# Optimization experiments

Measured on AMD Instinct MI355X. Metric: run time of the kernel, lower is better.

The kernel has to match this reference:

```python
import jax, jax.numpy as jnp
import numpy as np

N = 32768        # batch of sampled sequences
H = 1024         # LSTM hidden (cell) size
P = 128          # proj_size == output_size == operator_length
IN = 2 * (P + 1) + 4 + 1  # 263 = 2*(operator_length+1) + scatter_max_degree + 1
SOFT = 64        # soft_length
TSS = 16.0       # two_sigma_square
AZB, AZE = 0, 32    # operators.arity_zero_begin/end (token layout assumption)
A2B, A2E = 96, 128  # operators.arity_two_begin/end


def setup_inputs() -> dict:
    key = jax.random.key(0)
    ks = jax.random.split(key, 16)
    s = 0.05
    inp = {
        "input": jax.random.normal(ks[0], (N, IN), jnp.float32),
        "hidden": jax.random.normal(ks[1], (2, N, H), jnp.float32),       # c-state
        "hidden_lstm": jax.random.normal(ks[2], (2, N, P), jnp.float32),  # h-state (proj)
        # layer 0 (input -> H, projected to P)
        "W_ih0": jax.random.normal(ks[3], (4 * H, IN), jnp.float32) * s,
        "W_hh0": jax.random.normal(ks[4], (4 * H, P), jnp.float32) * s,
        "b_ih0": jax.random.normal(ks[5], (4 * H,), jnp.float32) * s,
        "b_hh0": jax.random.normal(ks[6], (4 * H,), jnp.float32) * s,
        "W_hr0": jax.random.normal(ks[7], (P, H), jnp.float32) * s,
        # layer 1 (P -> H, projected to P)
        "W_ih1": jax.random.normal(ks[8], (4 * H, P), jnp.float32) * s,
        "W_hh1": jax.random.normal(ks[9], (4 * H, P), jnp.float32) * s,
        "b_ih1": jax.random.normal(ks[10], (4 * H,), jnp.float32) * s,
        "b_hh1": jax.random.normal(ks[11], (4 * H,), jnp.float32) * s,
        "W_hr1": jax.random.normal(ks[12], (P, H), jnp.float32) * s,
        "cur_length": 10,
    }
    return inp


def lstm_cell(x, h, c, Wih, Whh, bih, bhh, Whr):
    # PyTorch gate order: i, f, g, o ; proj_size projection via Whr
    gates = x @ Wih.T + h @ Whh.T + (bih + bhh)   # [n, 4H]
    i, f, g, o = jnp.split(gates, 4, axis=-1)
    c_new = jax.nn.sigmoid(f) * c + jax.nn.sigmoid(i) * jnp.tanh(g)
    h_new = (jax.nn.sigmoid(o) * jnp.tanh(c_new)) @ Whr.T  # project H -> P
    return h_new, c_new


def reference(input, hidden, hidden_lstm,
              W_ih0, W_hh0, b_ih0, b_hh0, W_hr0,
              W_ih1, W_hh1, b_ih1, b_hh1, W_hr1,
              cur_length):
    h0, c0 = lstm_cell(input, hidden_lstm[0], hidden[0], W_ih0, W_hh0, b_ih0, b_hh0, W_hr0)
    h1, c1 = lstm_cell(h0, hidden_lstm[1], hidden[1], W_ih1, W_hh1, b_ih1, b_hh1, W_hr1)
    # prior bias (cur_length is a static Python int)
    prior = jnp.zeros((P,), jnp.float32)
    if cur_length < SOFT:
        prior = prior.at[AZB:AZE].set(-float(SOFT - cur_length) ** 2 / TSS)
    elif cur_length > SOFT:
        prior = prior.at[A2B:A2E].set(-float(cur_length - SOFT) ** 2 / TSS)
    out = jax.nn.softmax(h1 + prior[None, :], axis=1)  # [n, P]
    cn = jnp.stack([c0, c1])  # [2, n, H]
    hn = jnp.stack([h0, h1])  # [2, n, P]
    return out, cn, hn
```

## Files before the change

kernel.cpp:

```cpp
#include <hip/hip_runtime.h>
#include <stdint.h>

#define NB 32768
#define HH 1024
#define PP 128
#define INW 263
#define K0P 448
#define K1P 256
#define G4H 4096

typedef __attribute__((ext_vector_type(8))) short short8;
typedef __attribute__((ext_vector_type(4))) float floatx4;

__device__ __forceinline__ unsigned short f2bf(float x) {
    union { float f; unsigned int u; } v; v.f = x;
    unsigned int r = v.u + 0x7fffu + ((v.u >> 16) & 1u);
    return (unsigned short)(r >> 16);
}
__device__ __forceinline__ float sigm(float x) { return 1.f / (1.f + __expf(-x)); }
__device__ __forceinline__ float tanhfast(float x) { return 2.f / (1.f + __expf(-2.f * x)) - 1.f; }

__device__ __forceinline__ void load_lds16(const void* g, void* l) {
    __builtin_amdgcn_global_load_lds((const __attribute__((address_space(1))) void*)g,
                                     (__attribute__((address_space(3))) void*)l,
                                     16, 0, 0);
}

__global__ void prep_inputs(const float* __restrict__ inp, const float* __restrict__ hl,
                            unsigned short* __restrict__ X0, unsigned short* __restrict__ X1) {
    const int T0 = NB * K0P;
    const int T1 = T0 + NB * PP;
    for (int idx = blockIdx.x * 256 + threadIdx.x; idx < T1; idx += gridDim.x * 256) {
        if (idx < T0) {
            int n = idx / K0P, c = idx - n * K0P;
            float v = 0.f;
            if (c < INW) v = inp[n * INW + c];
            else if (c < INW + PP) v = hl[n * PP + (c - INW)];
            X0[idx] = f2bf(v);
        } else {
            int k = idx - T0;
            int n = k >> 7, c = k & 127;
            X1[n * K1P + PP + c] = f2bf(hl[NB * PP + k]);
        }
    }
}

__global__ void prep_weights(const float* __restrict__ Wih0, const float* __restrict__ Whh0,
                             const float* __restrict__ Wih1, const float* __restrict__ Whh1,
                             const float* __restrict__ Whr0, const float* __restrict__ Whr1,
                             const float* __restrict__ bih0, const float* __restrict__ bhh0,
                             const float* __restrict__ bih1, const float* __restrict__ bhh1,
                             unsigned short* __restrict__ Wp0, unsigned short* __restrict__ Wp1,
                             unsigned short* __restrict__ Whr0b, unsigned short* __restrict__ Whr1b,
                             float* __restrict__ b0, float* __restrict__ b1) {
    const int T0 = G4H * K0P;
    const int T1 = T0 + G4H * K1P;
    const int T2 = T1 + PP * HH;
    const int T3 = T2 + PP * HH;
    const int T4 = T3 + G4H;
    const int T5 = T4 + G4H;
    for (int idx = blockIdx.x * 256 + threadIdx.x; idx < T5; idx += gridDim.x * 256) {
        if (idx < T0) {
            int r = idx / K0P, c = idx - r * K0P;
            int cbb = r >> 7, tt = r & 127;
            int src = (tt >> 5) * 1024 + cbb * 32 + (tt & 31);
            float v = 0.f;
            if (c < INW) v = Wih0[src * INW + c];
            else if (c < INW + PP) v = Whh0[src * PP + (c - INW)];
            Wp0[idx] = f2bf(v);
        } else if (idx < T1) {
            int k = idx - T0;
            int r = k >> 8, c = k & 255;
            int cbb = r >> 7, tt = r & 127;
            int src = (tt >> 5) * 1024 + cbb * 32 + (tt & 31);
            float v = (c < PP) ? Wih1[src * PP + c] : Whh1[src * PP + (c - PP)];
            Wp1[k] = f2bf(v);
        } else if (idx < T2) {
            int k = idx - T1; Whr0b[k] = f2bf(Whr0[k]);
        } else if (idx < T3) {
            int k = idx - T2; Whr1b[k] = f2bf(Whr1[k]);
        } else if (idx < T4) {
            int k = idx - T3; b0[k] = bih0[k] + bhh0[k];
        } else {
            int k = idx - T4; b1[k] = bih1[k] + bhh1[k];
        }
    }
}

template<int KPAD>
__global__ __launch_bounds__(256, 2) void gemm_gates_k(
    const unsigned short* __restrict__ A,
    const unsigned short* __restrict__ Bp,
    const float* __restrict__ bias,
    const float* __restrict__ c_prev,
    float* __restrict__ c_out,
    unsigned short* __restrict__ tmp_out)
{
    __shared__ unsigned short As[128 * 64];
    __shared__ unsigned short Bs[128 * 64];
    const int t  = threadIdx.x;
    const int w  = t >> 6;
    const int l  = t & 63;
    const int lc = l & 15;
    const int q4 = l >> 4;
    const int cb = blockIdx.x;
    const int mb = blockIdx.y;

    floatx4 acc[2][8];
#pragma unroll
    for (int i = 0; i < 2; ++i)
#pragma unroll
        for (int j = 0; j < 8; ++j) acc[i][j] = (floatx4){0.f, 0.f, 0.f, 0.f};

    const int arow = t >> 3;
    const int sw   = ((t & 7) ^ ((t >> 3) & 7)) * 8;
    const unsigned short* gA = A  + (size_t)(mb * 128 + arow) * KPAD + sw;
    const unsigned short* gB = Bp + (size_t)(cb * 128 + arow) * KPAD + sw;
    char* ldsA = (char*)As + t * 16;
    char* ldsB = (char*)Bs + t * 16;

    for (int kt = 0; kt < KPAD; kt += 64) {
#pragma unroll
        for (int i = 0; i < 4; ++i) {
            load_lds16(gA + (size_t)(i * 32) * KPAD + kt, ldsA + i * 4096);
            load_lds16(gB + (size_t)(i * 32) * KPAD + kt, ldsB + i * 4096);
        }
        __syncthreads();
        const short* Asp = (const short*)As;
        const short* Bsp = (const short*)Bs;
#pragma unroll
        for (int kc = 0; kc < 2; ++kc) {
            const int kchunk = kc * 4 + q4;
            const int rsw = (kchunk ^ (lc & 7)) * 8;
            short8 a[2];
#pragma unroll
            for (int mi = 0; mi < 2; ++mi)
                a[mi] = *(const short8*)&Asp[(w * 32 + mi * 16 + lc) * 64 + rsw];
#pragma unroll
            for (int ci = 0; ci < 8; ++ci) {
                short8 b = *(const short8*)&Bsp[(ci * 16 + lc) * 64 + rsw];
#pragma unroll
                for (int mi = 0; mi < 2; ++mi)
                    acc[mi][ci] = __builtin_amdgcn_mfma_f32_16x16x32_bf16(a[mi], b, acc[mi][ci], 0, 0, 0);
            }
        }
        __syncthreads();
    }

#pragma unroll
    for (int u4 = 0; u4 < 2; ++u4) {
        const int hidx = cb * 32 + u4 * 16 + lc;
        const float bi = bias[hidx];
        const float bf = bias[1024 + hidx];
        const float bg = bias[2048 + hidx];
        const float bo = bias[3072 + hidx];
#pragma unroll
        for (int mi = 0; mi < 2; ++mi) {
#pragma unroll
            for (int r = 0; r < 4; ++r) {
                const int row = mb * 128 + w * 32 + mi * 16 + q4 * 4 + r;
                const float iv = acc[mi][0 + u4][r] + bi;
                const float fv = acc[mi][2 + u4][r] + bf;
                const float gv = acc[mi][4 + u4][r] + bg;
                const float ov = acc[mi][6 + u4][r] + bo;
                const float cp = c_prev[(size_t)row * 1024 + hidx];
                const float cn = sigm(fv) * cp + sigm(iv) * tanhfast(gv);
                c_out[(size_t)row * 1024 + hidx] = cn;
                tmp_out[(size_t)row * 1024 + hidx] = f2bf(sigm(ov) * tanhfast(cn));
            }
        }
    }
}

__global__ __launch_bounds__(256, 2) void gemm_proj_k(
    const unsigned short* __restrict__ A,
    const unsigned short* __restrict__ B,
    float* __restrict__ hout,
    unsigned short* __restrict__ xc1)
{
    __shared__ unsigned short As[128 * 64];
    __shared__ unsigned short Bs[128 * 64];
    const int t  = threadIdx.x;
    const int w  = t >> 6;
    const int l  = t & 63;
    const int lc = l & 15;
    const int q4 = l >> 4;
    const int mb = blockIdx.x;

    floatx4 acc[2][8];
#pragma unroll
    for (int i = 0; i < 2; ++i)
#pragma unroll
        for (int j = 0; j < 8; ++j) acc[i][j] = (floatx4){0.f, 0.f, 0.f, 0.f};

    const int arow = t >> 3;
    const int sw   = ((t & 7) ^ ((t >> 3) & 7)) * 8;
    const unsigned short* gA = A + (size_t)(mb * 128 + arow) * 1024 + sw;
    const unsigned short* gB = B + (size_t)arow * 1024 + sw;
    char* ldsA = (char*)As + t * 16;
    char* ldsB = (char*)Bs + t * 16;

    for (int kt = 0; kt < 1024; kt += 64) {
#pragma unroll
        for (int i = 0; i < 4; ++i) {
            load_lds16(gA + (size_t)(i * 32) * 1024 + kt, ldsA + i * 4096);
            load_lds16(gB + (size_t)(i * 32) * 1024 + kt, ldsB + i * 4096);
        }
        __syncthreads();
        const short* Asp = (const short*)As;
        const short* Bsp = (const short*)Bs;
#pragma unroll
        for (int kc = 0; kc < 2; ++kc) {
            const int kchunk = kc * 4 + q4;
            const int rsw = (kchunk ^ (lc & 7)) * 8;
            short8 a[2];
#pragma unroll
            for (int mi = 0; mi < 2; ++mi)
                a[mi] = *(const short8*)&Asp[(w * 32 + mi * 16 + lc) * 64 + rsw];
#pragma unroll
            for (int ci = 0; ci < 8; ++ci) {
                short8 b = *(const short8*)&Bsp[(ci * 16 + lc) * 64 + rsw];
#pragma unroll
                for (int mi = 0; mi < 2; ++mi)
                    acc[mi][ci] = __builtin_amdgcn_mfma_f32_16x16x32_bf16(a[mi], b, acc[mi][ci], 0, 0, 0);
            }
        }
        __syncthreads();
    }

#pragma unroll
    for (int ci = 0; ci < 8; ++ci) {
        const int col = ci * 16 + lc;
#pragma unroll
        for (int mi = 0; mi < 2; ++mi) {
#pragma unroll
            for (int r = 0; r < 4; ++r) {
                const int row = mb * 128 + w * 32 + mi * 16 + q4 * 4 + r;
                const float v = acc[mi][ci][r];
                hout[(size_t)row * 128 + col] = v;
                if (xc1) xc1[(size_t)row * K1P + col] = f2bf(v);
            }
        }
    }
}

__global__ void softmax_k(const float* __restrict__ h1, const int* __restrict__ clp,
                          float* __restrict__ out) {
    const int w = threadIdx.x >> 6, l = threadIdx.x & 63;
    const int row = blockIdx.x * 4 + w;
    const int cl = clp[0];
    float pd = 0.f;
    float d = (float)(64 - cl);
    float pv = -(d * d) * (1.f / 16.f);
    float p0 = (cl < 64 && l < 32) ? pv : 0.f;
    float p1 = (cl > 64 && (l + 64) >= 96) ? pv : 0.f;
    (void)pd;
    float v0 = h1[(size_t)row * 128 + l] + p0;
    float v1 = h1[(size_t)row * 128 + 64 + l] + p1;
    float m = fmaxf(v0, v1);
#pragma unroll
    for (int off = 32; off > 0; off >>= 1) m = fmaxf(m, __shfl_xor(m, off, 64));
    float e0 = __expf(v0 - m), e1 = __expf(v1 - m);
    float s = e0 + e1;
#pragma unroll
    for (int off = 32; off > 0; off >>= 1) s += __shfl_xor(s, off, 64);
    float inv = 1.f / s;
    out[(size_t)row * 128 + l] = e0 * inv;
    out[(size_t)row * 128 + 64 + l] = e1 * inv;
}

extern "C" void kernel_launch(void* const* d_in, const int* in_sizes, int n_in,
                              void* d_out, int out_size, void* d_ws, size_t ws_size,
                              hipStream_t stream) {
    const float* input = (const float*)d_in[0];
    const float* hidden = (const float*)d_in[1];
    const float* hlstm  = (const float*)d_in[2];
    const float* Wih0 = (const float*)d_in[3];
    const float* Whh0 = (const float*)d_in[4];
    const float* bih0 = (const float*)d_in[5];
    const float* bhh0 = (const float*)d_in[6];
    const float* Whr0 = (const float*)d_in[7];
    const float* Wih1 = (const float*)d_in[8];
    const float* Whh1 = (const float*)d_in[9];
    const float* bih1 = (const float*)d_in[10];
    const float* bhh1 = (const float*)d_in[11];
    const float* Whr1 = (const float*)d_in[12];
    const int* curlen = (const int*)d_in[13];

    float* out = (float*)d_out;
    float* cn0 = out + (size_t)NB * PP;
    float* cn1 = cn0 + (size_t)NB * HH;
    float* hn0 = cn1 + (size_t)NB * HH;
    float* hn1 = hn0 + (size_t)NB * PP;

    char* p = (char*)d_ws;
    unsigned short* X0    = (unsigned short*)p; p += (size_t)NB * K0P * 2;
    unsigned short* X1    = (unsigned short*)p; p += (size_t)NB * K1P * 2;
    unsigned short* Wp0   = (unsigned short*)p; p += (size_t)G4H * K0P * 2;
    unsigned short* Wp1   = (unsigned short*)p; p += (size_t)G4H * K1P * 2;
    unsigned short* Whr0b = (unsigned short*)p; p += (size_t)PP * HH * 2;
    unsigned short* Whr1b = (unsigned short*)p; p += (size_t)PP * HH * 2;
    float* b0 = (float*)p; p += (size_t)G4H * 4;
    float* b1 = (float*)p; p += (size_t)G4H * 4;
    unsigned short* tmp0 = (unsigned short*)p; p += (size_t)NB * HH * 2;
    unsigned short* tmp1 = (unsigned short*)p; p += (size_t)NB * HH * 2;

    prep_inputs<<<8192, 256, 0, stream>>>(input, hlstm, X0, X1);
    prep_weights<<<4096, 256, 0, stream>>>(Wih0, Whh0, Wih1, Whh1, Whr0, Whr1,
                                           bih0, bhh0, bih1, bhh1,
                                           Wp0, Wp1, Whr0b, Whr1b, b0, b1);
    gemm_gates_k<K0P><<<dim3(32, 256), 256, 0, stream>>>(X0, Wp0, b0, hidden, cn0, tmp0);
    gemm_proj_k<<<256, 256, 0, stream>>>(tmp0, Whr0b, hn0, X1);
    gemm_gates_k<K1P><<<dim3(32, 256), 256, 0, stream>>>(X1, Wp1, b1, hidden + (size_t)NB * HH, cn1, tmp1);
    gemm_proj_k<<<256, 256, 0, stream>>>(tmp1, Whr1b, hn1, nullptr);
    softmax_k<<<NB / 4, 256, 0, stream>>>(hn1, curlen, out);
}
```

Measured before the change: 913.8 us.

## Triple-buffer GEMM K-loops, enlarge gate tiles, shrink proj tiles, restructure prep kernels

The gate GEMM now uses 256x128 tiles and a 3-stage ring of 32-wide K slices, waiting on vmcnt instead of a full barrier, so global loads overlap MFMA work. It also prefetches c_prev and bias before the last K steps. The projection GEMM drops to 64-row tiles (512 blocks) with the same 3-stage pipeline to give more blocks for parallelism. The prep kernels switch from flat grid-stride indexing with divisions to per-row blocks. The cost is higher register and LDS pressure from the 4x8 accumulators, and the hand-written waitcnt counts must stay exactly in step with the number of loads issued per stage.

Result: no change. 906.9 us (-0.8%).

```diff
diff --git a/kernel.cpp b/kernel.cpp
--- a/kernel.cpp
+++ b/kernel.cpp
@@ -28,19 +28,19 @@
 
 __global__ void prep_inputs(const float* __restrict__ inp, const float* __restrict__ hl,
                             unsigned short* __restrict__ X0, unsigned short* __restrict__ X1) {
-    const int T0 = NB * K0P;
-    const int T1 = T0 + NB * PP;
-    for (int idx = blockIdx.x * 256 + threadIdx.x; idx < T1; idx += gridDim.x * 256) {
-        if (idx < T0) {
-            int n = idx / K0P, c = idx - n * K0P;
+    const int n0 = blockIdx.x * 4;
+#pragma unroll
+    for (int rr = 0; rr < 4; ++rr) {
+        const int n = n0 + rr;
+        for (int c = threadIdx.x; c < K0P; c += 256) {
             float v = 0.f;
             if (c < INW) v = inp[n * INW + c];
             else if (c < INW + PP) v = hl[n * PP + (c - INW)];
-            X0[idx] = f2bf(v);
-        } else {
-            int k = idx - T0;
-            int n = k >> 7, c = k & 127;
-            X1[n * K1P + PP + c] = f2bf(hl[NB * PP + k]);
+            X0[(size_t)n * K0P + c] = f2bf(v);
+        }
+        if (threadIdx.x < PP) {
+            const int c = threadIdx.x;
+            X1[(size_t)n * K1P + PP + c] = f2bf(hl[(size_t)NB * PP + n * PP + c]);
         }
     }
 }
@@ -53,37 +53,29 @@
                              unsigned short* __restrict__ Wp0, unsigned short* __restrict__ Wp1,
                              unsigned short* __restrict__ Whr0b, unsigned short* __restrict__ Whr1b,
                              float* __restrict__ b0, float* __restrict__ b1) {
-    const int T0 = G4H * K0P;
-    const int T1 = T0 + G4H * K1P;
-    const int T2 = T1 + PP * HH;
-    const int T3 = T2 + PP * HH;
-    const int T4 = T3 + G4H;
-    const int T5 = T4 + G4H;
-    for (int idx = blockIdx.x * 256 + threadIdx.x; idx < T5; idx += gridDim.x * 256) {
-        if (idx < T0) {
-            int r = idx / K0P, c = idx - r * K0P;
-            int cbb = r >> 7, tt = r & 127;
-            int src = (tt >> 5) * 1024 + cbb * 32 + (tt & 31);
-            float v = 0.f;
-            if (c < INW) v = Wih0[src * INW + c];
-            else if (c < INW + PP) v = Whh0[src * PP + (c - INW)];
-            Wp0[idx] = f2bf(v);
-        } else if (idx < T1) {
-            int k = idx - T0;
-            int r = k >> 8, c = k & 255;
-            int cbb = r >> 7, tt = r & 127;
-            int src = (tt >> 5) * 1024 + cbb * 32 + (tt & 31);
-            float v = (c < PP) ? Wih1[src * PP + c] : Whh1[src * PP + (c - PP)];
-            Wp1[k] = f2bf(v);
-        } else if (idx < T2) {
-            int k = idx - T1; Whr0b[k] = f2bf(Whr0[k]);
-        } else if (idx < T3) {
-            int k = idx - T2; Whr1b[k] = f2bf(Whr1[k]);
-        } else if (idx < T4) {
-            int k = idx - T3; b0[k] = bih0[k] + bhh0[k];
-        } else {
-            int k = idx - T4; b1[k] = bih1[k] + bhh1[k];
-        }
+    const int b = blockIdx.x;
+    const int cbb = b >> 7, tt = b & 127;
+    const int src = (tt >> 5) * 1024 + cbb * 32 + (tt & 31);
+    for (int c = threadIdx.x; c < K0P; c += 256) {
+        float v = 0.f;
+        if (c < INW) v = Wih0[src * INW + c];
+        else if (c < INW + PP) v = Whh0[src * PP + (c - INW)];
+        Wp0[(size_t)b * K0P + c] = f2bf(v);
+    }
+    for (int c = threadIdx.x; c < K1P; c += 256) {
+        float v = (c < PP) ? Wih1[src * PP + c] : Whh1[src * PP + (c - PP)];
+        Wp1[(size_t)b * K1P + c] = f2bf(v);
+    }
+    if (b < PP) {
+        for (int c = threadIdx.x; c < HH; c += 256) {
+            Whr0b[b * HH + c] = f2bf(Whr0[b * HH + c]);
+            Whr1b[b * HH + c] = f2bf(Whr1[b * HH + c]);
+        }
+    }
+    if (b < 16) {
+        const int k = b * 256 + threadIdx.x;
+        b0[k] = bih0[k] + bhh0[k];
+        b1[k] = bih1[k] + bhh1[k];
     }
 }
 
@@ -96,8 +88,8 @@
     float* __restrict__ c_out,
     unsigned short* __restrict__ tmp_out)
 {
-    __shared__ unsigned short As[128 * 64];
-    __shared__ unsigned short Bs[128 * 64];
+    __shared__ unsigned short As[3 * 256 * 32];
+    __shared__ unsigned short Bs[3 * 128 * 32];
     const int t  = threadIdx.x;
     const int w  = t >> 6;
     const int l  = t & 63;
@@ -106,64 +98,99 @@
     const int cb = blockIdx.x;
     const int mb = blockIdx.y;
 
-    floatx4 acc[2][8];
-#pragma unroll
-    for (int i = 0; i < 2; ++i)
+    floatx4 acc[4][8];
+#pragma unroll
+    for (int i = 0; i < 4; ++i)
 #pragma unroll
         for (int j = 0; j < 8; ++j) acc[i][j] = (floatx4){0.f, 0.f, 0.f, 0.f};
 
-    const int arow = t >> 3;
-    const int sw   = ((t & 7) ^ ((t >> 3) & 7)) * 8;
-    const unsigned short* gA = A  + (size_t)(mb * 128 + arow) * KPAD + sw;
-    const unsigned short* gB = Bp + (size_t)(cb * 128 + arow) * KPAD + sw;
-    char* ldsA = (char*)As + t * 16;
-    char* ldsB = (char*)Bs + t * 16;
-
-    for (int kt = 0; kt < KPAD; kt += 64) {
-#pragma unroll
-        for (int i = 0; i < 4; ++i) {
-            load_lds16(gA + (size_t)(i * 32) * KPAD + kt, ldsA + i * 4096);
-            load_lds16(gB + (size_t)(i * 32) * KPAD + kt, ldsB + i * 4096);
-        }
-        __syncthreads();
-        const short* Asp = (const short*)As;
-        const short* Bsp = (const short*)Bs;
-#pragma unroll
-        for (int kc = 0; kc < 2; ++kc) {
-            const int kchunk = kc * 4 + q4;
-            const int rsw = (kchunk ^ (lc & 7)) * 8;
-            short8 a[2];
-#pragma unroll
-            for (int mi = 0; mi < 2; ++mi)
-                a[mi] = *(const short8*)&Asp[(w * 32 + mi * 16 + lc) * 64 + rsw];
-#pragma unroll
-            for (int ci = 0; ci < 8; ++ci) {
-                short8 b = *(const short8*)&Bsp[(ci * 16 + lc) * 64 + rsw];
-#pragma unroll
-                for (int mi = 0; mi < 2; ++mi)
-                    acc[mi][ci] = __builtin_amdgcn_mfma_f32_16x16x32_bf16(a[mi], b, acc[mi][ci], 0, 0, 0);
+    const int ar = t >> 2;
+    const int aj = (t & 3) ^ ((t >> 3) & 3);
+    const unsigned short* gA = A  + (size_t)(mb * 256 + ar) * KPAD + aj * 8;
+    const unsigned short* gB = Bp + (size_t)(cb * 128 + ar) * KPAD + aj * 8;
+    char* lA = (char*)As + t * 16;
+    char* lB = (char*)Bs + t * 16;
+
+#define GSTAGE(buf, kte) do {                                                       \
+    _Pragma("unroll") for (int i_ = 0; i_ < 4; ++i_)                                \
+        load_lds16(gA + (size_t)(i_ * 64) * KPAD + (kte), lA + (buf) * 16384 + i_ * 4096); \
+    _Pragma("unroll") for (int i_ = 0; i_ < 2; ++i_)                                \
+        load_lds16(gB + (size_t)(i_ * 64) * KPAD + (kte), lB + (buf) * 8192 + i_ * 4096);  \
+} while (0)
+
+    constexpr int NT = KPAD / 32;
+
+    GSTAGE(0, 0);
+    GSTAGE(1, 32);
+    GSTAGE(2, 64);
+
+    float cpv[4][2][4];
+    float bv[2][4];
+
+#pragma unroll
+    for (int ki = 0; ki < NT; ++ki) {
+        if (ki < NT - 2)       asm volatile("s_waitcnt vmcnt(12)" ::: "memory");
+        else if (ki == NT - 2) asm volatile("s_waitcnt vmcnt(6)" ::: "memory");
+        else                   asm volatile("s_waitcnt vmcnt(0)" ::: "memory");
+
+        if (ki == NT - 2) {
+#pragma unroll
+            for (int u4 = 0; u4 < 2; ++u4) {
+                const int hidx = cb * 32 + u4 * 16 + lc;
+#pragma unroll
+                for (int j = 0; j < 4; ++j) bv[u4][j] = bias[j * 1024 + hidx];
+#pragma unroll
+                for (int mi = 0; mi < 4; ++mi)
+#pragma unroll
+                    for (int r = 0; r < 4; ++r)
+                        cpv[mi][u4][r] =
+                            c_prev[(size_t)(mb * 256 + w * 64 + mi * 16 + q4 * 4 + r) * 1024 + hidx];
             }
         }
-        __syncthreads();
-    }
+
+        __builtin_amdgcn_s_barrier();
+        asm volatile("" ::: "memory");
+
+        const short* Asp = (const short*)As + (ki % 3) * 8192;
+        const short* Bsp = (const short*)Bs + (ki % 3) * 4096;
+        const int pos8 = (q4 ^ ((lc >> 1) & 3)) * 8;
+        short8 a[4];
+#pragma unroll
+        for (int mi = 0; mi < 4; ++mi)
+            a[mi] = *(const short8*)&Asp[(w * 64 + mi * 16 + lc) * 32 + pos8];
+#pragma unroll
+        for (int ci = 0; ci < 8; ++ci) {
+            short8 b = *(const short8*)&Bsp[(ci * 16 + lc) * 32 + pos8];
+#pragma unroll
+            for (int mi = 0; mi < 4; ++mi)
+                acc[mi][ci] = __builtin_amdgcn_mfma_f32_16x16x32_bf16(a[mi], b, acc[mi][ci], 0, 0, 0);
+        }
+
+        if (ki + 3 < NT) {
+            asm volatile("" ::: "memory");
+            __builtin_amdgcn_s_barrier();
+            GSTAGE(ki % 3, (ki + 3) * 32);
+        }
+    }
+#undef GSTAGE
 
 #pragma unroll
     for (int u4 = 0; u4 < 2; ++u4) {
         const int hidx = cb * 32 + u4 * 16 + lc;
-        const float bi = bias[hidx];
-        const float bf = bias[1024 + hidx];
-        const float bg = bias[2048 + hidx];
-        const float bo = bias[3072 + hidx];
-#pragma unroll
-        for (int mi = 0; mi < 2; ++mi) {
+        const float bi = bv[u4][0];
+        const float bf = bv[u4][1];
+        const float bg = bv[u4][2];
+        const float bo = bv[u4][3];
+#pragma unroll
+        for (int mi = 0; mi < 4; ++mi) {
 #pragma unroll
             for (int r = 0; r < 4; ++r) {
-                const int row = mb * 128 + w * 32 + mi * 16 + q4 * 4 + r;
+                const int row = mb * 256 + w * 64 + mi * 16 + q4 * 4 + r;
                 const float iv = acc[mi][0 + u4][r] + bi;
                 const float fv = acc[mi][2 + u4][r] + bf;
                 const float gv = acc[mi][4 + u4][r] + bg;
                 const float ov = acc[mi][6 + u4][r] + bo;
-                const float cp = c_prev[(size_t)row * 1024 + hidx];
+                const float cp = cpv[mi][u4][r];
                 const float cn = sigm(fv) * cp + sigm(iv) * tanhfast(gv);
                 c_out[(size_t)row * 1024 + hidx] = cn;
                 tmp_out[(size_t)row * 1024 + hidx] = f2bf(sigm(ov) * tanhfast(cn));
@@ -178,8 +205,8 @@
     float* __restrict__ hout,
     unsigned short* __restrict__ xc1)
 {
-    __shared__ unsigned short As[128 * 64];
-    __shared__ unsigned short Bs[128 * 64];
+    __shared__ unsigned short As[3 * 64 * 32];
+    __shared__ unsigned short Bs[3 * 128 * 32];
     const int t  = threadIdx.x;
     const int w  = t >> 6;
     const int l  = t & 63;
@@ -187,59 +214,64 @@
     const int q4 = l >> 4;
     const int mb = blockIdx.x;
 
-    floatx4 acc[2][8];
-#pragma unroll
-    for (int i = 0; i < 2; ++i)
-#pragma unroll
-        for (int j = 0; j < 8; ++j) acc[i][j] = (floatx4){0.f, 0.f, 0.f, 0.f};
-
-    const int arow = t >> 3;
-    const int sw   = ((t & 7) ^ ((t >> 3) & 7)) * 8;
-    const unsigned short* gA = A + (size_t)(mb * 128 + arow) * 1024 + sw;
-    const unsigned short* gB = B + (size_t)arow * 1024 + sw;
-    char* ldsA = (char*)As + t * 16;
-    char* ldsB = (char*)Bs + t * 16;
-
-    for (int kt = 0; kt < 1024; kt += 64) {
-#pragma unroll
-        for (int i = 0; i < 4; ++i) {
-            load_lds16(gA + (size_t)(i * 32) * 1024 + kt, ldsA + i * 4096);
-            load_lds16(gB + (size_t)(i * 32) * 1024 + kt, ldsB + i * 4096);
-        }
-        __syncthreads();
-        const short* Asp = (const short*)As;
-        const short* Bsp = (const short*)Bs;
-#pragma unroll
-        for (int kc = 0; kc < 2; ++kc) {
-            const int kchunk = kc * 4 + q4;
-            const int rsw = (kchunk ^ (lc & 7)) * 8;
-            short8 a[2];
-#pragma unroll
-            for (int mi = 0; mi < 2; ++mi)
-                a[mi] = *(const short8*)&Asp[(w * 32 + mi * 16 + lc) * 64 + rsw];
-#pragma unroll
-            for (int ci = 0; ci < 8; ++ci) {
-                short8 b = *(const short8*)&Bsp[(ci * 16 + lc) * 64 + rsw];
-#pragma unroll
-                for (int mi = 0; mi < 2; ++mi)
-                    acc[mi][ci] = __builtin_amdgcn_mfma_f32_16x16x32_bf16(a[mi], b, acc[mi][ci], 0, 0, 0);
-            }
-        }
-        __syncthreads();
-    }
+    floatx4 acc[8];
+#pragma unroll
+    for (int j = 0; j < 8; ++j) acc[j] = (floatx4){0.f, 0.f, 0.f, 0.f};
+
+    const int ar = t >> 2;
+    const int aj = (t & 3) ^ ((t >> 3) & 3);
+    const unsigned short* gA = A + (size_t)(mb * 64 + ar) * 1024 + aj * 8;
+    const unsigned short* gB = B + (size_t)ar * 1024 + aj * 8;
+    char* lA = (char*)As + t * 16;
+    char* lB = (char*)Bs + t * 16;
+
+#define PSTAGE(buf, kte) do {                                                      \
+    load_lds16(gA + (kte), lA + (buf) * 4096);                                     \
+    _Pragma("unroll") for (int i_ = 0; i_ < 2; ++i_)                               \
+        load_lds16(gB + (size_t)(i_ * 64) * 1024 + (kte), lB + (buf) * 8192 + i_ * 4096); \
+} while (0)
+
+    constexpr int NT = 32;
+
+    PSTAGE(0, 0);
+    PSTAGE(1, 32);
+    PSTAGE(2, 64);
+
+#pragma unroll
+    for (int ki = 0; ki < NT; ++ki) {
+        if (ki < NT - 2)       asm volatile("s_waitcnt vmcnt(6)" ::: "memory");
+        else if (ki == NT - 2) asm volatile("s_waitcnt vmcnt(3)" ::: "memory");
+        else                   asm volatile("s_waitcnt vmcnt(0)" ::: "memory");
+        __builtin_amdgcn_s_barrier();
+        asm volatile("" ::: "memory");
+
+        const short* Asp = (const short*)As + (ki % 3) * 2048;
+        const short* Bsp = (const short*)Bs + (ki % 3) * 4096;
+        const int pos8 = (q4 ^ ((lc >> 1) & 3)) * 8;
+        short8 a = *(const short8*)&Asp[(w * 16 + lc) * 32 + pos8];
+#pragma unroll
+        for (int ci = 0; ci < 8; ++ci) {
+            short8 b = *(const short8*)&Bsp[(ci * 16 + lc) * 32 + pos8];
+            acc[ci] = __builtin_amdgcn_mfma_f32_16x16x32_bf16(a, b, acc[ci], 0, 0, 0);
+        }
+
+        if (ki + 3 < NT) {
+            asm volatile("" ::: "memory");
+            __builtin_amdgcn_s_barrier();
+            PSTAGE(ki % 3, (ki + 3) * 32);
+        }
+    }
+#undef PSTAGE
 
 #pragma unroll
     for (int ci = 0; ci < 8; ++ci) {
         const int col = ci * 16 + lc;
 #pragma unroll
-        for (int mi = 0; mi < 2; ++mi) {
-#pragma unroll
-            for (int r = 0; r < 4; ++r) {
-                const int row = mb * 128 + w * 32 + mi * 16 + q4 * 4 + r;
-                const float v = acc[mi][ci][r];
-                hout[(size_t)row * 128 + col] = v;
-                if (xc1) xc1[(size_t)row * K1P + col] = f2bf(v);
-            }
+        for (int r = 0; r < 4; ++r) {
+            const int row = mb * 64 + w * 16 + q4 * 4 + r;
+            const float v = acc[ci][r];
+            hout[(size_t)row * 128 + col] = v;
+            if (xc1) xc1[(size_t)row * K1P + col] = f2bf(v);
         }
     }
 }
@@ -249,12 +281,10 @@
     const int w = threadIdx.x >> 6, l = threadIdx.x & 63;
     const int row = blockIdx.x * 4 + w;
     const int cl = clp[0];
-    float pd = 0.f;
     float d = (float)(64 - cl);
     float pv = -(d * d) * (1.f / 16.f);
     float p0 = (cl < 64 && l < 32) ? pv : 0.f;
     float p1 = (cl > 64 && (l + 64) >= 96) ? pv : 0.f;
-    (void)pd;
     float v0 = h1[(size_t)row * 128 + l] + p0;
     float v1 = h1[(size_t)row * 128 + 64 + l] + p1;
     float m = fmaxf(v0, v1);
@@ -305,13 +335,13 @@
     unsigned short* tmp0 = (unsigned short*)p; p += (size_t)NB * HH * 2;
     unsigned short* tmp1 = (unsigned short*)p; p += (size_t)NB * HH * 2;
 
-    prep_inputs<<<8192, 256, 0, stream>>>(input, hlstm, X0, X1);
-    prep_weights<<<4096, 256, 0, stream>>>(Wih0, Whh0, Wih1, Whh1, Whr0, Whr1,
-                                           bih0, bhh0, bih1, bhh1,
-                                           Wp0, Wp1, Whr0b, Whr1b, b0, b1);
-    gemm_gates_k<K0P><<<dim3(32, 256), 256, 0, stream>>>(X0, Wp0, b0, hidden, cn0, tmp0);
-    gemm_proj_k<<<256, 256, 0, stream>>>(tmp0, Whr0b, hn0, X1);
-    gemm_gates_k<K1P><<<dim3(32, 256), 256, 0, stream>>>(X1, Wp1, b1, hidden + (size_t)NB * HH, cn1, tmp1);
-    gemm_proj_k<<<256, 256, 0, stream>>>(tmp1, Whr1b, hn1, nullptr);
+    prep_inputs<<<NB / 4, 256, 0, stream>>>(input, hlstm, X0, X1);
+    prep_weights<<<G4H, 256, 0, stream>>>(Wih0, Whh0, Wih1, Whh1, Whr0, Whr1,
+                                          bih0, bhh0, bih1, bhh1,
+                                          Wp0, Wp1, Whr0b, Whr1b, b0, b1);
+    gemm_gates_k<K0P><<<dim3(32, 128), 256, 0, stream>>>(X0, Wp0, b0, hidden, cn0, tmp0);
+    gemm_proj_k<<<512, 256, 0, stream>>>(tmp0, Whr0b, hn0, X1);
+    gemm_gates_k<K1P><<<dim3(32, 128), 256, 0, stream>>>(X1, Wp1, b1, hidden + (size_t)NB * HH, cn1, tmp1);
+    gemm_proj_k<<<512, 256, 0, stream>>>(tmp1, Whr1b, hn1, nullptr);
     softmax_k<<<NB / 4, 256, 0, stream>>>(hn1, curlen, out);
 }
```
